# Kernel optimization log

Hardware: AMD Instinct MI355X
Metric: run time of the kernel (lower is better)

## Reference

```python
import jax, jax.numpy as jnp
import numpy as np

U, I, D = 100000, 50000, 64
N = U + I
E_G, E_U, E_I = 2400000, 1600000, 800000


def _spmm(rows, cols, vals, x, n):
    # sparse [n, m] @ dense [m, d] via gather + scale + segment-sum scatter
    return jax.ops.segment_sum(x[cols] * vals[:, None], rows, num_segments=n)


def setup_inputs() -> dict:
    key = jax.random.key(0)
    ks = jax.random.split(key, 11)
    return {
        "user_emb": jax.random.normal(ks[0], (U, D), dtype=jnp.float32),
        "item_emb": jax.random.normal(ks[1], (I, D), dtype=jnp.float32),
        "graph_rows": jax.random.randint(ks[2], (E_G,), 0, N, dtype=jnp.int32),
        "graph_cols": jax.random.randint(ks[3], (E_G,), 0, N, dtype=jnp.int32),
        "graph_vals": jax.random.uniform(ks[4], (E_G,), dtype=jnp.float32),
        "user_rows": jax.random.randint(ks[5], (E_U,), 0, U, dtype=jnp.int32),
        "user_cols": jax.random.randint(ks[6], (E_U,), 0, U, dtype=jnp.int32),
        "user_vals": jax.random.uniform(ks[7], (E_U,), dtype=jnp.float32),
        "item_rows": jax.random.randint(ks[8], (E_I,), 0, I, dtype=jnp.int32),
        "item_cols": jax.random.randint(ks[9], (E_I,), 0, I, dtype=jnp.int32),
        "item_vals": jax.random.uniform(ks[10], (E_I,), dtype=jnp.float32),
    }


def reference(user_emb, item_emb,
              graph_rows, graph_cols, graph_vals,
              user_rows, user_cols, user_vals,
              item_rows, item_cols, item_vals):
    all_emb = jnp.concatenate([user_emb, item_emb], axis=0)  # [N, D]
    all_emb1 = _spmm(graph_rows, graph_cols, graph_vals, all_emb, N)
    user_emb2 = _spmm(user_rows, user_cols, user_vals, user_emb, U)
    item_emb2 = _spmm(item_rows, item_cols, item_vals, item_emb, I)
    user_emb1, item_emb1 = all_emb1[:U], all_emb1[U:]
    return (user_emb1, item_emb1, user_emb2, item_emb2)
```

## Files before the change

kernel.cpp:

```cpp
#include <hip/hip_runtime.h>

#define DDIM 64
constexpr int U_CNT = 100000;
constexpr int I_CNT = 50000;
constexpr int N_CNT = U_CNT + I_CNT;
constexpr int NB    = N_CNT + U_CNT + I_CNT;

constexpr int BIN_ROWS_LOG = 7;
constexpr int BIN_ROWS = 1 << BIN_ROWS_LOG;
constexpr int BINS = (NB + BIN_ROWS - 1) / BIN_ROWS;
constexpr int BINS_PAD = 2560;
constexpr int SORT_EDGES = 4096;
constexpr int HIST_EDGES = 16384;
constexpr int CAP = 2432;
constexpr int CAPH = 1536;
constexpr int NSLOT = 5;

constexpr int SB_LOG = 12;
constexpr int NSB = (NB + (1 << SB_LOG) - 1) >> SB_LOG;
constexpr int NSB_PAD = 128;
constexpr int CAP_SB = 67584;
constexpr int MAXCH = (CAP_SB + SORT_EDGES - 1) / SORT_EDGES;
constexpr int BWIN = 80;
constexpr int BWIN_PAD = 128;

typedef unsigned u32x2 __attribute__((ext_vector_type(2)));
typedef unsigned u32x4 __attribute__((ext_vector_type(4)));
typedef float    f32x2 __attribute__((ext_vector_type(2)));

__device__ __forceinline__ int wave_incl_scan(int v, int lane) {
#pragma unroll
    for (int off = 1; off < 64; off <<= 1) {
        int t = __shfl_up(v, off, 64);
        if (lane >= off) v += t;
    }
    return v;
}

__device__ __forceinline__ unsigned short f2bf_rne(float f) {
    unsigned u = __float_as_uint(f);
    unsigned r = (u + 0x7FFFu + ((u >> 16) & 1u)) >> 16;
    return (unsigned short)r;
}

__global__ __launch_bounds__(1024) void init_cursors(int* __restrict__ sbcur,
                                                     int* __restrict__ bincur) {
    int i = blockIdx.x * 1024 + threadIdx.x;
    if (i < NSB) sbcur[i] = i * CAP_SB;
    if (i < BINS) bincur[i] = i * CAP;
}

__global__ __launch_bounds__(256) void convert_emb(const float* __restrict__ ue,
                                                   const float* __restrict__ ie,
                                                   unsigned short* __restrict__ emb16) {
    int g = blockIdx.x * 256 + threadIdx.x;
    constexpr int UG = U_CNT * (DDIM / 4);
    constexpr int TG = N_CNT * (DDIM / 4);
    if (g >= TG) return;
    float4 v = (g < UG) ? ((const float4*)ue)[g] : ((const float4*)ie)[g - UG];
    ushort4 o;
    o.x = f2bf_rne(v.x); o.y = f2bf_rne(v.y); o.z = f2bf_rne(v.z); o.w = f2bf_rne(v.w);
    ((ushort4*)emb16)[g] = o;
}

__global__ __launch_bounds__(1024) void hist_conv(const int* __restrict__ gr,
                                                  const int* __restrict__ ur,
                                                  const int* __restrict__ ir,
                                                  int EG, int EU, int EI,
                                                  int* __restrict__ cnt,
                                                  const float* __restrict__ ue,
                                                  const float* __restrict__ ie,
                                                  unsigned short* __restrict__ emb16) {
    __shared__ int h[BINS_PAD];
    for (int i = threadIdx.x; i < BINS_PAD; i += 1024) h[i] = 0;
    if (emb16) {
        constexpr int UG = U_CNT * (DDIM / 4);
        constexpr int TG = N_CNT * (DDIM / 4);
        int stride = (int)gridDim.x * 1024;
        for (int g = blockIdx.x * 1024 + threadIdx.x; g < TG; g += stride) {
            float4 v = (g < UG) ? ((const float4*)ue)[g] : ((const float4*)ie)[g - UG];
            ushort4 o;
            o.x = f2bf_rne(v.x); o.y = f2bf_rne(v.y); o.z = f2bf_rne(v.z); o.w = f2bf_rne(v.w);
            ((ushort4*)emb16)[g] = o;
        }
    }
    __syncthreads();
    int base = blockIdx.x * HIST_EDGES;
    int Et = EG + EU + EI;
    for (int j = 0; j < HIST_EDGES / 1024; ++j) {
        int e = base + j * 1024 + threadIdx.x;
        if (e < Et) {
            int b;
            if (e < EG)           b = gr[e];
            else if (e < EG + EU) b = N_CNT + ur[e - EG];
            else                  b = N_CNT + U_CNT + ir[e - EG - EU];
            atomicAdd(&h[b >> BIN_ROWS_LOG], 1);
        }
    }
    __syncthreads();
    for (int i = threadIdx.x; i < BINS; i += 1024) {
        int v = h[i];
        if (v) atomicAdd(&cnt[i], v);
    }
}

__global__ __launch_bounds__(1024) void scan_bins(const int* __restrict__ cnt,
                                                  int* __restrict__ bin_base,
                                                  int* __restrict__ bin_cursor,
                                                  int* __restrict__ sb_base,
                                                  int* __restrict__ sb_cursor,
                                                  int E_total) {
    __shared__ int wsum[16], woff[16];
    int tid = threadIdx.x, lane = tid & 63, wid = tid >> 6;
    int i0 = 3 * tid, i1 = i0 + 1, i2 = i0 + 2;
    int c0 = (i0 < BINS) ? cnt[i0] : 0;
    int c1 = (i1 < BINS) ? cnt[i1] : 0;
    int c2 = (i2 < BINS) ? cnt[i2] : 0;
    int v = c0 + c1 + c2;
    int incl = wave_incl_scan(v, lane);
    if (lane == 63) wsum[wid] = incl;
    __syncthreads();
    if (wid == 0 && lane < 16) {
        int s = wsum[lane], si = s;
#pragma unroll
        for (int off = 1; off < 16; off <<= 1) {
            int t = __shfl_up(si, off, 64);
            if (lane >= off) si += t;
        }
        woff[lane] = si - s;
    }
    __syncthreads();
    int e = incl - v + woff[wid];
    if (i0 < BINS) { bin_base[i0] = e;           bin_cursor[i0] = e; }
    if (i1 < BINS) { bin_base[i1] = e + c0;      bin_cursor[i1] = e + c0; }
    if (i2 < BINS) { bin_base[i2] = e + c0 + c1; bin_cursor[i2] = e + c0 + c1; }
    if (tid == 0) bin_base[BINS] = E_total;
    __syncthreads();
    if (tid <= NSB) {
        int idx = tid << (SB_LOG - BIN_ROWS_LOG);
        int vv = (idx >= BINS) ? E_total : bin_base[idx];
        sb_base[tid] = vv;
        if (tid < NSB) sb_cursor[tid] = vv;
    }
}

__global__ __launch_bounds__(512, 8) void sbsort_all(
        const int* __restrict__ gr, const int* __restrict__ gc, const float* __restrict__ gv,
        const int* __restrict__ ur, const int* __restrict__ uc, const float* __restrict__ uv,
        const int* __restrict__ ir, const int* __restrict__ ic, const float* __restrict__ iv,
        int EG, int EU, int EI,
        int* __restrict__ sb_cursor, uint2* __restrict__ poolA) {
    __shared__ uint2 sorted[SORT_EDGES];
    __shared__ unsigned char ssb[SORT_EDGES];
    __shared__ int hist[NSB_PAD];
    __shared__ int lscan[NSB_PAD];
    __shared__ int lcur[NSB_PAD];
    __shared__ int wsum2[2];

    int tid = threadIdx.x, lane = tid & 63, wid = tid >> 6;
    for (int i = tid; i < NSB_PAD; i += 512) { hist[i] = 0; lcur[i] = 0; }
    __syncthreads();

    const int Et = EG + EU + EI;
    int start = blockIdx.x * SORT_EDGES;
    int base_e = start + tid * 8;
    int myb[8]; unsigned mylo[8]; float myv[8];

#pragma unroll
    for (int j = 0; j < 8; j += 4) {
        int e = base_e + j;
        int sg0 = (e < EG) ? 0 : (e < EG + EU ? 1 : 2);
        int sg3 = (e + 3 < EG) ? 0 : (e + 3 < EG + EU ? 1 : 2);
        if (e + 3 < Et && sg0 == sg3) {
            const int* R; const int* Cc; const float* V; int boff, goff, loc;
            if (sg0 == 0)      { R = gr; Cc = gc; V = gv; boff = 0;             goff = 0;     loc = e; }
            else if (sg0 == 1) { R = ur; Cc = uc; V = uv; boff = N_CNT;         goff = 0;     loc = e - EG; }
            else               { R = ir; Cc = ic; V = iv; boff = N_CNT + U_CNT; goff = U_CNT; loc = e - EG - EU; }
            int4   r4 = *(const int4*)(R + loc);
            int4   c4 = *(const int4*)(Cc + loc);
            float4 v4 = *(const float4*)(V + loc);
            int rr[4] = {r4.x, r4.y, r4.z, r4.w};
            int cc[4] = {c4.x, c4.y, c4.z, c4.w};
            float vv[4] = {v4.x, v4.y, v4.z, v4.w};
#pragma unroll
            for (int q = 0; q < 4; ++q) {
                int bucket = boff + rr[q];
                int sb = bucket >> SB_LOG;
                myb[j + q] = sb;
                mylo[j + q] = ((unsigned)(bucket & 4095) << 18) | (unsigned)(goff + cc[q]);
                myv[j + q] = vv[q];
                atomicAdd(&hist[sb], 1);
            }
        } else {
#pragma unroll
            for (int q = 0; q < 4; ++q) {
                int ee = e + q;
                if (ee < Et) {
                    int r, c; float vl; int boff, goff;
                    if (ee < EG)           { r = gr[ee]; c = gc[ee]; vl = gv[ee]; boff = 0; goff = 0; }
                    else if (ee < EG + EU) { int k = ee - EG;      r = ur[k]; c = uc[k]; vl = uv[k]; boff = N_CNT;         goff = 0; }
                    else                   { int k = ee - EG - EU; r = ir[k]; c = ic[k]; vl = iv[k]; boff = N_CNT + U_CNT; goff = U_CNT; }
                    int bucket = boff + r;
                    int sb = bucket >> SB_LOG;
                    myb[j + q] = sb;
                    mylo[j + q] = ((unsigned)(bucket & 4095) << 18) | (unsigned)(goff + c);
                    myv[j + q] = vl;
                    atomicAdd(&hist[sb], 1);
                } else myb[j + q] = -1;
            }
        }
    }
    __syncthreads();

    int v = 0, incl = 0;
    if (tid < NSB_PAD) {
        v = hist[tid];
        incl = wave_incl_scan(v, lane);
        if (lane == 63) wsum2[wid] = incl;
    }
    __syncthreads();
    if (tid < NSB_PAD) {
        int st = incl - v + (wid ? wsum2[0] : 0);
        lscan[tid] = st;
        if (tid < NSB && v) hist[tid] = atomicAdd(&sb_cursor[tid], v);
    }
    __syncthreads();

#pragma unroll
    for (int j = 0; j < 8; ++j) {
        if (myb[j] >= 0) {
            int p = lscan[myb[j]] + atomicAdd(&lcur[myb[j]], 1);
            sorted[p] = make_uint2(mylo[j], __float_as_uint(myv[j]));
            ssb[p] = (unsigned char)myb[j];
        }
    }
    __syncthreads();

    int cntE = min(SORT_EDGES, Et - start);
    for (int pos = tid; pos < cntE; pos += 512) {
        int b = ssb[pos];
        uint2 t = sorted[pos];
        u32x2 q; q.x = t.x; q.y = t.y;
        __builtin_nontemporal_store(q, (u32x2*)&poolA[hist[b] + (pos - lscan[b])]);
    }
}

__global__ __launch_bounds__(512, 8) void binsort2_fx(const uint2* __restrict__ poolA,
                                                      const int* __restrict__ sbcur,
                                                      int* __restrict__ bincur,
                                                      uint2* __restrict__ poolB) {
    __shared__ uint2 sorted[SORT_EDGES];
    __shared__ unsigned char sbin[SORT_EDGES];
    __shared__ int hist[32], lscan[32], lcur[32];

    int sb = blockIdx.y, c = blockIdx.x;
    int cnt_sb = sbcur[sb] - sb * CAP_SB;
    int lo = c * SORT_EDGES;
    if (lo >= cnt_sb) return;
    int m = min(SORT_EDGES, cnt_sb - lo);

    int tid = threadIdx.x, lane = tid & 63;
    if (tid < 32) hist[tid] = 0;
    __syncthreads();

    const uint2* src = poolA + (size_t)sb * CAP_SB + lo;
    int base = tid * 8;
    int mys[8]; uint2 myp[8];
#pragma unroll
    for (int j = 0; j < 8; j += 2) {
        int e = base + j;
        uint2 p0, p1;
        bool v1 = (e + 1 < m), v0 = (e < m);
        if (v1) {
            u32x4 q = __builtin_nontemporal_load((const u32x4*)(src + e));
            p0.x = q.x; p0.y = q.y; p1.x = q.z; p1.y = q.w;
        } else if (v0) {
            u32x2 q = __builtin_nontemporal_load((const u32x2*)(src + e));
            p0.x = q.x; p0.y = q.y;
        }
        if (v0) {
            int slot = (int)(p0.x >> 25);
            mys[j] = slot; myp[j] = p0;
            atomicAdd(&hist[slot], 1);
        } else mys[j] = -1;
        if (v1) {
            int slot = (int)(p1.x >> 25);
            mys[j + 1] = slot; myp[j + 1] = p1;
            atomicAdd(&hist[slot], 1);
        } else mys[j + 1] = -1;
    }
    __syncthreads();

    if (tid < 64) {
        int vv = (tid < 32) ? hist[tid] : 0;
        int incl = wave_incl_scan(vv, lane);
        if (tid < 32) { lscan[tid] = incl - vv; lcur[tid] = incl - vv; }
    }
    __syncthreads();
    if (tid < 32 && hist[tid] > 0)
        hist[tid] = atomicAdd(&bincur[(sb << 5) + tid], hist[tid]);
    __syncthreads();

#pragma unroll
    for (int j = 0; j < 8; ++j) {
        if (mys[j] >= 0) {
            int p = atomicAdd(&lcur[mys[j]], 1);
            sorted[p] = myp[j];
            sbin[p] = (unsigned char)mys[j];
        }
    }
    __syncthreads();

    for (int pos = tid; pos < m; pos += 512) {
        int sl = sbin[pos];
        uint2 t = sorted[pos];
        u32x2 q; q.x = t.x; q.y = t.y;
        __builtin_nontemporal_store(q, (u32x2*)&poolB[hist[sl] + (pos - lscan[sl])]);
    }
}

__global__ __launch_bounds__(512, 8) void binsort2_win(const uint2* __restrict__ poolA,
                                                       const int* __restrict__ sb_base, int Et,
                                                       int* __restrict__ bin_cursor,
                                                       uint2* __restrict__ poolB) {
    __shared__ uint2 sorted[SORT_EDGES];
    __shared__ unsigned char sbin[SORT_EDGES];
    __shared__ int hist[BWIN_PAD];
    __shared__ int lscan[BWIN_PAD];
    __shared__ int lcur[BWIN_PAD];
    __shared__ int ssbb[NSB + 1];
    __shared__ int wsum2[2];
    __shared__ int sblo_s, nloc;

    int tid = threadIdx.x, lane = tid & 63, wid = tid >> 6;
    if (tid < BWIN_PAD) hist[tid] = 0;
    if (tid <= NSB) ssbb[tid] = sb_base[tid];
    __syncthreads();

    int start = blockIdx.x * SORT_EDGES;
    int base_e = start + tid * 8;
    int sb;
    {
        int lo2 = 0, hi2 = NSB - 1;
        while (lo2 < hi2) {
            int mid = (lo2 + hi2 + 1) >> 1;
            if (ssbb[mid] <= base_e) lo2 = mid; else hi2 = mid - 1;
        }
        sb = lo2;
    }
    if (tid == 0) {
        int lo2 = 0, hi2 = NSB - 1;
        while (lo2 < hi2) {
            int mid = (lo2 + hi2 + 1) >> 1;
            if (ssbb[mid] <= start) lo2 = mid; else hi2 = mid - 1;
        }
        sblo_s = lo2;
    }
    __syncthreads();
    int sb_lo = sblo_s;
    int W0 = sb_lo << (SB_LOG - BIN_ROWS_LOG);

    int myb[8]; uint2 myp[8];
#pragma unroll
    for (int j = 0; j < 8; j += 2) {
        int e = base_e + j;
        uint2 p0, p1;
        bool v1 = (e + 1 < Et), v0 = (e < Et);
        if (v1) {
            u32x4 q = __builtin_nontemporal_load((const u32x4*)(poolA + e));
            p0.x = q.x; p0.y = q.y; p1.x = q.z; p1.y = q.w;
        } else if (v0) {
            u32x2 q = __builtin_nontemporal_load((const u32x2*)(poolA + e));
            p0.x = q.x; p0.y = q.y;
        }
        if (v0) {
            while (sb < NSB - 1 && e >= ssbb[sb + 1]) ++sb;
            int slot = ((sb - sb_lo) << (SB_LOG - BIN_ROWS_LOG)) + (int)(p0.x >> 25);
            if ((unsigned)slot < (unsigned)BWIN) {
                myb[j] = slot; myp[j] = p0;
                atomicAdd(&hist[slot], 1);
            } else {
                int b = (sb << (SB_LOG - BIN_ROWS_LOG)) + (int)(p0.x >> 25);
                int gp = atomicAdd(&bin_cursor[b], 1);
                poolB[gp] = p0;
                myb[j] = -1;
            }
        } else myb[j] = -1;
        if (v1) {
            int e1 = e + 1;
            while (sb < NSB - 1 && e1 >= ssbb[sb + 1]) ++sb;
            int slot = ((sb - sb_lo) << (SB_LOG - BIN_ROWS_LOG)) + (int)(p1.x >> 25);
            if ((unsigned)slot < (unsigned)BWIN) {
                myb[j + 1] = slot; myp[j + 1] = p1;
                atomicAdd(&hist[slot], 1);
            } else {
                int b = (sb << (SB_LOG - BIN_ROWS_LOG)) + (int)(p1.x >> 25);
                int gp = atomicAdd(&bin_cursor[b], 1);
                poolB[gp] = p1;
                myb[j + 1] = -1;
            }
        } else myb[j + 1] = -1;
    }
    __syncthreads();

    int v = 0, incl = 0;
    if (tid < BWIN_PAD) {
        v = hist[tid];
        incl = wave_incl_scan(v, lane);
        if (lane == 63) wsum2[wid] = incl;
    }
    __syncthreads();
    if (tid < BWIN_PAD) {
        int st = incl - v + (wid ? wsum2[0] : 0);
        lscan[tid] = st; lcur[tid] = st;
        if (tid == BWIN_PAD - 1) nloc = st + v;
    }
    __syncthreads();
    if (tid < BWIN && hist[tid] > 0)
        hist[tid] = atomicAdd(&bin_cursor[W0 + tid], hist[tid]);
    __syncthreads();

#pragma unroll
    for (int j = 0; j < 8; ++j) {
        if (myb[j] >= 0) {
            int p = atomicAdd(&lcur[myb[j]], 1);
            sorted[p] = myp[j];
            sbin[p] = (unsigned char)myb[j];
        }
    }
    __syncthreads();

    int tot = nloc;
    for (int pos = tid; pos < tot; pos += 512) {
        int sl = sbin[pos];
        uint2 t = sorted[pos];
        u32x2 q; q.x = t.x; q.y = t.y;
        __builtin_nontemporal_store(q, (u32x2*)&poolB[hist[sl] + (pos - lscan[sl])]);
    }
}

__global__ __launch_bounds__(512, 8) void refine_accum(const int* __restrict__ bin_base,
                                                       const int* __restrict__ bincur,
                                                       const uint2* __restrict__ pool,
                                                       const unsigned short* __restrict__ emb16,
                                                       float* __restrict__ out) {
    __shared__ uint2 sorted[CAPH + 4];
    __shared__ int rhist[BIN_ROWS];
    __shared__ int rstart[BIN_ROWS];
    __shared__ int rcur[BIN_ROWS];
    __shared__ int wsum[2];
    int tid = threadIdx.x, lane = tid & 63, wid = tid >> 6;

    int ix = (int)blockIdx.x;
    int b = ix >> 1;
    int rlo = (ix & 1) << 6, rhi = rlo + 64;

    int s, cnt;
    if (bin_base) { s = bin_base[b]; cnt = min(bin_base[b + 1] - s, CAP); }
    else          { s = b * CAP;     cnt = min(bincur[b] - s, CAP); }

    if (tid < BIN_ROWS) rhist[tid] = 0;
    __syncthreads();

    uint2 my[NSLOT];
    const u32x2* poolv = (const u32x2*)(pool + s);
#pragma unroll
    for (int j = 0; j < NSLOT; ++j) {
        int idx = tid + j * 512;
        if (idx < cnt) {
            u32x2 q = __builtin_nontemporal_load(poolv + idx);
            my[j].x = q.x; my[j].y = q.y;
            int rl = (int)((q.x >> 18) & 127u);
            if (rl >= rlo && rl < rhi) atomicAdd(&rhist[rl], 1);
        }
    }
    __syncthreads();

    int v = 0, incl = 0;
    if (tid < BIN_ROWS) {
        v = rhist[tid];
        incl = wave_incl_scan(v, lane);
        if (lane == 63) wsum[wid] = incl;
    }
    __syncthreads();
    if (tid < BIN_ROWS) {
        int st = incl - v + (wid ? wsum[0] : 0);
        rstart[tid] = st; rcur[tid] = st;
    }
    __syncthreads();

#pragma unroll
    for (int j = 0; j < NSLOT; ++j) {
        int idx = tid + j * 512;
        if (idx < cnt) {
            int rl = (int)((my[j].x >> 18) & 127u);
            if (rl >= rlo && rl < rhi) {
                int pos = atomicAdd(&rcur[rl], 1);
                if (pos < CAPH) sorted[pos] = my[j];
            }
        }
    }
    __syncthreads();
    if (tid == 0) {
        int total = rcur[rhi - 1];
        if (total > CAPH) total = CAPH;
        sorted[total] = make_uint2(0u, 0u);
    }
    __syncthreads();

    long long rowbase = (long long)b * BIN_ROWS;
    int half = lane >> 5, hl = lane & 31;
    const unsigned* emb32 = (const unsigned*)emb16;
    for (int r = rlo + wid; r < rhi; r += 8) {
        long long row = rowbase + r;
        if (row >= NB) break;
        int k = rstart[r], ke = k + rhist[r];
        float a0 = 0.f, a1 = 0.f, c0 = 0.f, c1 = 0.f;
        for (; k + 8 <= ke; k += 8) {
            uint2 p0 = sorted[k + half];
            uint2 p1 = sorted[k + 2 + half];
            uint2 p2 = sorted[k + 4 + half];
            uint2 p3 = sorted[k + 6 + half];
            unsigned w0 = emb32[((size_t)(p0.x & 0x3FFFFu) << 5) + hl];
            unsigned w1 = emb32[((size_t)(p1.x & 0x3FFFFu) << 5) + hl];
            unsigned w2 = emb32[((size_t)(p2.x & 0x3FFFFu) << 5) + hl];
            unsigned w3 = emb32[((size_t)(p3.x & 0x3FFFFu) << 5) + hl];
            float v0 = __uint_as_float(p0.y), v1 = __uint_as_float(p1.y);
            float v2 = __uint_as_float(p2.y), v3 = __uint_as_float(p3.y);
            a0 += v0 * __uint_as_float(w0 << 16);
            a1 += v0 * __uint_as_float(w0 & 0xFFFF0000u);
            c0 += v1 * __uint_as_float(w1 << 16);
            c1 += v1 * __uint_as_float(w1 & 0xFFFF0000u);
            a0 += v2 * __uint_as_float(w2 << 16);
            a1 += v2 * __uint_as_float(w2 & 0xFFFF0000u);
            c0 += v3 * __uint_as_float(w3 << 16);
            c1 += v3 * __uint_as_float(w3 & 0xFFFF0000u);
        }
        for (; k + 2 <= ke; k += 2) {
            uint2 p = sorted[k + half];
            unsigned w = emb32[((size_t)(p.x & 0x3FFFFu) << 5) + hl];
            float vv = __uint_as_float(p.y);
            a0 += vv * __uint_as_float(w << 16);
            a1 += vv * __uint_as_float(w & 0xFFFF0000u);
        }
        if (k < ke) {
            uint2 p = sorted[k + half];
            unsigned w = emb32[((size_t)(p.x & 0x3FFFFu) << 5) + hl];
            float vv = half ? 0.f : __uint_as_float(p.y);
            a0 += vv * __uint_as_float(w << 16);
            a1 += vv * __uint_as_float(w & 0xFFFF0000u);
        }
        a0 += c0; a1 += c1;
        a0 += __shfl_xor(a0, 32, 64);
        a1 += __shfl_xor(a1, 32, 64);
        if (lane < 32) {
            f32x2 o; o.x = a0; o.y = a1;
            __builtin_nontemporal_store(o, (f32x2*)(out + (size_t)row * DDIM + 2 * hl));
        }
    }
}

__global__ void spmm_graph_kernel(const int* __restrict__ rows, const int* __restrict__ cols,
                                  const float* __restrict__ vals,
                                  const float* __restrict__ user_emb,
                                  const float* __restrict__ item_emb,
                                  float* __restrict__ out, int E) {
    long long idx = (long long)blockIdx.x * blockDim.x + threadIdx.x;
    int e = (int)(idx >> 6), d = (int)(idx & 63);
    if (e >= E) return;
    int r = rows[e], c = cols[e];
    float v = vals[e];
    float x = (c < U_CNT) ? user_emb[(long long)c * DDIM + d]
                          : item_emb[(long long)(c - U_CNT) * DDIM + d];
    atomicAdd(&out[(long long)r * DDIM + d], v * x);
}

__global__ void spmm_plain_kernel(const int* __restrict__ rows, const int* __restrict__ cols,
                                  const float* __restrict__ vals,
                                  const float* __restrict__ emb,
                                  float* __restrict__ out, int E) {
    long long idx = (long long)blockIdx.x * blockDim.x + threadIdx.x;
    int e = (int)(idx >> 6), d = (int)(idx & 63);
    if (e >= E) return;
    int r = rows[e], c = cols[e];
    atomicAdd(&out[(long long)r * DDIM + d], vals[e] * emb[(long long)c * DDIM + d]);
}

extern "C" void kernel_launch(void* const* d_in, const int* in_sizes, int n_in,
                              void* d_out, int out_size, void* d_ws, size_t ws_size,
                              hipStream_t stream) {
    const float* user_emb = (const float*)d_in[0];
    const float* item_emb = (const float*)d_in[1];
    const int*   g_rows   = (const int*)d_in[2];
    const int*   g_cols   = (const int*)d_in[3];
    const float* g_vals   = (const float*)d_in[4];
    const int*   u_rows   = (const int*)d_in[5];
    const int*   u_cols   = (const int*)d_in[6];
    const float* u_vals   = (const float*)d_in[7];
    const int*   i_rows   = (const int*)d_in[8];
    const int*   i_cols   = (const int*)d_in[9];
    const float* i_vals   = (const float*)d_in[10];
    float* out = (float*)d_out;

    const int EG = in_sizes[2];
    const int EU = in_sizes[5];
    const int EI = in_sizes[8];
    const int Et = EG + EU + EI;

    const size_t emb_bytes = (size_t)N_CNT * DDIM * sizeof(unsigned short);
    unsigned cgrid = (unsigned)((N_CNT * (DDIM / 4) + 255) / 256);

    size_t f_off_bc  = 80 * sizeof(int);
    size_t f_off_pa  = (f_off_bc + (size_t)BINS * sizeof(int) + 127) & ~(size_t)127;
    size_t f_pa_sz   = (size_t)NSB * CAP_SB * sizeof(uint2);
    size_t f_off_pb  = (f_off_pa + f_pa_sz + 127) & ~(size_t)127;
    size_t f_pb_sz   = (size_t)BINS * CAP * sizeof(uint2);
    size_t needed_fx = f_off_pb + f_pb_sz;

    size_t t_off_bb   = (size_t)BINS_PAD * sizeof(int);
    size_t t_off_bc   = t_off_bb + (size_t)(BINS + 1) * sizeof(int);
    size_t t_off_sbb  = t_off_bc + (size_t)BINS * sizeof(int);
    size_t t_off_sbc  = t_off_sbb + (size_t)(NSB + 1) * sizeof(int);
    size_t t_off_pa   = (t_off_sbc + (size_t)NSB * sizeof(int) + 127) & ~(size_t)127;
    size_t t_off_pb   = (t_off_pa + (size_t)Et * sizeof(uint2) + 127) & ~(size_t)127;
    size_t needed_2p  = t_off_pb + (size_t)Et * sizeof(uint2);
    size_t t_off_emb  = (needed_2p + 127) & ~(size_t)127;
    size_t needed_na  = t_off_emb + emb_bytes;
    bool pa_fits_emb  = (size_t)Et * sizeof(uint2) >= emb_bytes;

    if (ws_size >= needed_fx && f_pa_sz >= emb_bytes) {
        int*   sbcur  = (int*)d_ws;
        int*   bincur = (int*)((char*)d_ws + f_off_bc);
        uint2* poolA  = (uint2*)((char*)d_ws + f_off_pa);
        uint2* poolB  = (uint2*)((char*)d_ws + f_off_pb);
        unsigned short* emb16 = (unsigned short*)poolA;

        init_cursors<<<3, 1024, 0, stream>>>(sbcur, bincur);

        unsigned nb2 = (unsigned)((Et + SORT_EDGES - 1) / SORT_EDGES);
        sbsort_all<<<nb2, 512, 0, stream>>>(g_rows, g_cols, g_vals,
                                            u_rows, u_cols, u_vals,
                                            i_rows, i_cols, i_vals,
                                            EG, EU, EI, sbcur, poolA);
        binsort2_fx<<<dim3(MAXCH, NSB), 512, 0, stream>>>(poolA, sbcur, bincur, poolB);
        convert_emb<<<cgrid, 256, 0, stream>>>(user_emb, item_emb, emb16);
        refine_accum<<<2 * BINS, 512, 0, stream>>>(nullptr, bincur, poolB, emb16, out);
    } else if (ws_size >= needed_2p && pa_fits_emb) {
        bool noalias = (ws_size >= needed_na);
        int*   cnt        = (int*)d_ws;
        int*   bin_base   = (int*)((char*)d_ws + t_off_bb);
        int*   bin_cursor = (int*)((char*)d_ws + t_off_bc);
        int*   sb_base    = (int*)((char*)d_ws + t_off_sbb);
        int*   sb_cursor  = (int*)((char*)d_ws + t_off_sbc);
        uint2* poolA      = (uint2*)((char*)d_ws + t_off_pa);
        uint2* poolB      = (uint2*)((char*)d_ws + t_off_pb);
        unsigned short* emb16 = noalias ? (unsigned short*)((char*)d_ws + t_off_emb)
                                        : (unsigned short*)poolA;

        hipMemsetAsync(cnt, 0, (size_t)BINS_PAD * sizeof(int), stream);
        unsigned hblocks = (unsigned)((Et + HIST_EDGES - 1) / HIST_EDGES);
        hist_conv<<<hblocks, 1024, 0, stream>>>(g_rows, u_rows, i_rows, EG, EU, EI, cnt,
                                                user_emb, item_emb,
                                                noalias ? emb16 : (unsigned short*)nullptr);
        scan_bins<<<1, 1024, 0, stream>>>(cnt, bin_base, bin_cursor, sb_base, sb_cursor, Et);

        unsigned nb2 = (unsigned)((Et + SORT_EDGES - 1) / SORT_EDGES);
        sbsort_all<<<nb2, 512, 0, stream>>>(g_rows, g_cols, g_vals,
                                            u_rows, u_cols, u_vals,
                                            i_rows, i_cols, i_vals,
                                            EG, EU, EI, sb_cursor, poolA);
        binsort2_win<<<nb2, 512, 0, stream>>>(poolA, sb_base, Et, bin_cursor, poolB);

        if (!noalias)
            convert_emb<<<cgrid, 256, 0, stream>>>(user_emb, item_emb, emb16);

        refine_accum<<<2 * BINS, 512, 0, stream>>>(bin_base, nullptr, poolB, emb16, out);
    } else {
        hipMemsetAsync(d_out, 0, (size_t)out_size * sizeof(float), stream);
        const int block = 256;
        {
            long long t = (long long)EG * DDIM;
            spmm_graph_kernel<<<(unsigned)((t + block - 1) / block), block, 0, stream>>>(
                g_rows, g_cols, g_vals, user_emb, item_emb, out, EG);
        }
        {
            long long t = (long long)EU * DDIM;
            spmm_plain_kernel<<<(unsigned)((t + block - 1) / block), block, 0, stream>>>(
                u_rows, u_cols, u_vals, user_emb, out + (size_t)N_CNT * DDIM, EU);
        }
        {
            long long t = (long long)EI * DDIM;
            spmm_plain_kernel<<<(unsigned)((t + block - 1) / block), block, 0, stream>>>(
                i_rows, i_cols, i_vals, item_emb, out + (size_t)(N_CNT + U_CNT) * DDIM, EI);
        }
    }
}
```

Baseline: 323.5 us.

## Fuse bf16 embedding conversion into sort kernel and use 1024-thread blocks

```diff
diff --git a/kernel.cpp b/kernel.cpp
--- a/kernel.cpp
+++ b/kernel.cpp
@@ -13,8 +13,7 @@
 constexpr int SORT_EDGES = 4096;
 constexpr int HIST_EDGES = 16384;
 constexpr int CAP = 2432;
-constexpr int CAPH = 1536;
-constexpr int NSLOT = 5;
+constexpr int NSLOT = 3;
 
 constexpr int SB_LOG = 12;
 constexpr int NSB = (NB + (1 << SB_LOG) - 1) >> SB_LOG;
@@ -144,12 +143,14 @@
     }
 }
 
-__global__ __launch_bounds__(512, 8) void sbsort_all(
+__global__ __launch_bounds__(1024, 8) void sbsort_all(
         const int* __restrict__ gr, const int* __restrict__ gc, const float* __restrict__ gv,
         const int* __restrict__ ur, const int* __restrict__ uc, const float* __restrict__ uv,
         const int* __restrict__ ir, const int* __restrict__ ic, const float* __restrict__ iv,
         int EG, int EU, int EI,
-        int* __restrict__ sb_cursor, uint2* __restrict__ poolA) {
+        int* __restrict__ sb_cursor, uint2* __restrict__ poolA,
+        const float* __restrict__ ue, const float* __restrict__ ie,
+        unsigned short* __restrict__ emb16c) {
     __shared__ uint2 sorted[SORT_EDGES];
     __shared__ unsigned char ssb[SORT_EDGES];
     __shared__ int hist[NSB_PAD];
@@ -158,17 +159,16 @@
     __shared__ int wsum2[2];
 
     int tid = threadIdx.x, lane = tid & 63, wid = tid >> 6;
-    for (int i = tid; i < NSB_PAD; i += 512) { hist[i] = 0; lcur[i] = 0; }
+    if (tid < NSB_PAD) { hist[tid] = 0; lcur[tid] = 0; }
     __syncthreads();
 
     const int Et = EG + EU + EI;
     int start = blockIdx.x * SORT_EDGES;
-    int base_e = start + tid * 8;
-    int myb[8]; unsigned mylo[8]; float myv[8];
-
-#pragma unroll
-    for (int j = 0; j < 8; j += 4) {
-        int e = base_e + j;
+    int base_e = start + tid * 4;
+    int myb[4]; unsigned mylo[4]; float myv[4];
+
+    {
+        int e = base_e;
         int sg0 = (e < EG) ? 0 : (e < EG + EU ? 1 : 2);
         int sg3 = (e + 3 < EG) ? 0 : (e + 3 < EG + EU ? 1 : 2);
         if (e + 3 < Et && sg0 == sg3) {
@@ -186,9 +186,9 @@
             for (int q = 0; q < 4; ++q) {
                 int bucket = boff + rr[q];
                 int sb = bucket >> SB_LOG;
-                myb[j + q] = sb;
-                mylo[j + q] = ((unsigned)(bucket & 4095) << 18) | (unsigned)(goff + cc[q]);
-                myv[j + q] = vv[q];
+                myb[q] = sb;
+                mylo[q] = ((unsigned)(bucket & 4095) << 18) | (unsigned)(goff + cc[q]);
+                myv[q] = vv[q];
                 atomicAdd(&hist[sb], 1);
             }
         } else {
@@ -202,11 +202,11 @@
                     else                   { int k = ee - EG - EU; r = ir[k]; c = ic[k]; vl = iv[k]; boff = N_CNT + U_CNT; goff = U_CNT; }
                     int bucket = boff + r;
                     int sb = bucket >> SB_LOG;
-                    myb[j + q] = sb;
-                    mylo[j + q] = ((unsigned)(bucket & 4095) << 18) | (unsigned)(goff + c);
-                    myv[j + q] = vl;
+                    myb[q] = sb;
+                    mylo[q] = ((unsigned)(bucket & 4095) << 18) | (unsigned)(goff + c);
+                    myv[q] = vl;
                     atomicAdd(&hist[sb], 1);
-                } else myb[j + q] = -1;
+                } else myb[q] = -1;
             }
         }
     }
@@ -227,7 +227,7 @@
     __syncthreads();
 
 #pragma unroll
-    for (int j = 0; j < 8; ++j) {
+    for (int j = 0; j < 4; ++j) {
         if (myb[j] >= 0) {
             int p = lscan[myb[j]] + atomicAdd(&lcur[myb[j]], 1);
             sorted[p] = make_uint2(mylo[j], __float_as_uint(myv[j]));
@@ -237,18 +237,30 @@
     __syncthreads();
 
     int cntE = min(SORT_EDGES, Et - start);
-    for (int pos = tid; pos < cntE; pos += 512) {
+    for (int pos = tid; pos < cntE; pos += 1024) {
         int b = ssb[pos];
         uint2 t = sorted[pos];
         u32x2 q; q.x = t.x; q.y = t.y;
         __builtin_nontemporal_store(q, (u32x2*)&poolA[hist[b] + (pos - lscan[b])]);
     }
-}
-
-__global__ __launch_bounds__(512, 8) void binsort2_fx(const uint2* __restrict__ poolA,
-                                                      const int* __restrict__ sbcur,
-                                                      int* __restrict__ bincur,
-                                                      uint2* __restrict__ poolB) {
+
+    if (emb16c) {
+        constexpr int UG = U_CNT * (DDIM / 4);
+        constexpr int TG = N_CNT * (DDIM / 4);
+        int stride = (int)gridDim.x * 1024;
+        for (int g = blockIdx.x * 1024 + tid; g < TG; g += stride) {
+            float4 vv = (g < UG) ? ((const float4*)ue)[g] : ((const float4*)ie)[g - UG];
+            ushort4 o;
+            o.x = f2bf_rne(vv.x); o.y = f2bf_rne(vv.y); o.z = f2bf_rne(vv.z); o.w = f2bf_rne(vv.w);
+            ((ushort4*)emb16c)[g] = o;
+        }
+    }
+}
+
+__global__ __launch_bounds__(1024, 8) void binsort2_fx(const uint2* __restrict__ poolA,
+                                                       const int* __restrict__ sbcur,
+                                                       int* __restrict__ bincur,
+                                                       uint2* __restrict__ poolB) {
     __shared__ uint2 sorted[SORT_EDGES];
     __shared__ unsigned char sbin[SORT_EDGES];
     __shared__ int hist[32], lscan[32], lcur[32];
@@ -264,10 +276,10 @@
     __syncthreads();
 
     const uint2* src = poolA + (size_t)sb * CAP_SB + lo;
-    int base = tid * 8;
-    int mys[8]; uint2 myp[8];
-#pragma unroll
-    for (int j = 0; j < 8; j += 2) {
+    int base = tid * 4;
+    int mys[4]; uint2 myp[4];
+#pragma unroll
+    for (int j = 0; j < 4; j += 2) {
         int e = base + j;
         uint2 p0, p1;
         bool v1 = (e + 1 < m), v0 = (e < m);
@@ -302,7 +314,7 @@
     __syncthreads();
 
 #pragma unroll
-    for (int j = 0; j < 8; ++j) {
+    for (int j = 0; j < 4; ++j) {
         if (mys[j] >= 0) {
             int p = atomicAdd(&lcur[mys[j]], 1);
             sorted[p] = myp[j];
@@ -311,7 +323,7 @@
     }
     __syncthreads();
 
-    for (int pos = tid; pos < m; pos += 512) {
+    for (int pos = tid; pos < m; pos += 1024) {
         int sl = sbin[pos];
         uint2 t = sorted[pos];
         u32x2 q; q.x = t.x; q.y = t.y;
@@ -439,22 +451,19 @@
     }
 }
 
-__global__ __launch_bounds__(512, 8) void refine_accum(const int* __restrict__ bin_base,
-                                                       const int* __restrict__ bincur,
-                                                       const uint2* __restrict__ pool,
-                                                       const unsigned short* __restrict__ emb16,
-                                                       float* __restrict__ out) {
-    __shared__ uint2 sorted[CAPH + 4];
+__global__ __launch_bounds__(1024, 8) void refine_accum(const int* __restrict__ bin_base,
+                                                        const int* __restrict__ bincur,
+                                                        const uint2* __restrict__ pool,
+                                                        const unsigned short* __restrict__ emb16,
+                                                        float* __restrict__ out) {
+    __shared__ uint2 sorted[CAP + 2];
     __shared__ int rhist[BIN_ROWS];
     __shared__ int rstart[BIN_ROWS];
     __shared__ int rcur[BIN_ROWS];
     __shared__ int wsum[2];
     int tid = threadIdx.x, lane = tid & 63, wid = tid >> 6;
 
-    int ix = (int)blockIdx.x;
-    int b = ix >> 1;
-    int rlo = (ix & 1) << 6, rhi = rlo + 64;
-
+    int b = (int)blockIdx.x;
     int s, cnt;
     if (bin_base) { s = bin_base[b]; cnt = min(bin_base[b + 1] - s, CAP); }
     else          { s = b * CAP;     cnt = min(bincur[b] - s, CAP); }
@@ -466,12 +475,11 @@
     const u32x2* poolv = (const u32x2*)(pool + s);
 #pragma unroll
     for (int j = 0; j < NSLOT; ++j) {
-        int idx = tid + j * 512;
+        int idx = tid + j * 1024;
         if (idx < cnt) {
             u32x2 q = __builtin_nontemporal_load(poolv + idx);
             my[j].x = q.x; my[j].y = q.y;
-            int rl = (int)((q.x >> 18) & 127u);
-            if (rl >= rlo && rl < rhi) atomicAdd(&rhist[rl], 1);
+            atomicAdd(&rhist[(q.x >> 18) & 127u], 1);
         }
     }
     __syncthreads();
@@ -491,27 +499,20 @@
 
 #pragma unroll
     for (int j = 0; j < NSLOT; ++j) {
-        int idx = tid + j * 512;
+        int idx = tid + j * 1024;
         if (idx < cnt) {
-            int rl = (int)((my[j].x >> 18) & 127u);
-            if (rl >= rlo && rl < rhi) {
-                int pos = atomicAdd(&rcur[rl], 1);
-                if (pos < CAPH) sorted[pos] = my[j];
-            }
-        }
-    }
-    __syncthreads();
-    if (tid == 0) {
-        int total = rcur[rhi - 1];
-        if (total > CAPH) total = CAPH;
-        sorted[total] = make_uint2(0u, 0u);
-    }
+            int pos = atomicAdd(&rcur[(my[j].x >> 18) & 127u], 1);
+            sorted[pos] = my[j];
+        }
+    }
+    __syncthreads();
+    if (tid == 0) sorted[cnt] = make_uint2(0u, 0u);
     __syncthreads();
 
     long long rowbase = (long long)b * BIN_ROWS;
     int half = lane >> 5, hl = lane & 31;
     const unsigned* emb32 = (const unsigned*)emb16;
-    for (int r = rlo + wid; r < rhi; r += 8) {
+    for (int r = wid; r < BIN_ROWS; r += 16) {
         long long row = rowbase + r;
         if (row >= NB) break;
         int k = rstart[r], ke = k + rhist[r];
@@ -610,12 +611,17 @@
     const size_t emb_bytes = (size_t)N_CNT * DDIM * sizeof(unsigned short);
     unsigned cgrid = (unsigned)((N_CNT * (DDIM / 4) + 255) / 256);
 
-    size_t f_off_bc  = 80 * sizeof(int);
-    size_t f_off_pa  = (f_off_bc + (size_t)BINS * sizeof(int) + 127) & ~(size_t)127;
-    size_t f_pa_sz   = (size_t)NSB * CAP_SB * sizeof(uint2);
-    size_t f_off_pb  = (f_off_pa + f_pa_sz + 127) & ~(size_t)127;
-    size_t f_pb_sz   = (size_t)BINS * CAP * sizeof(uint2);
-    size_t needed_fx = f_off_pb + f_pb_sz;
+    size_t f_off_bc   = 80 * sizeof(int);
+    size_t f_hdr_end  = f_off_bc + (size_t)BINS * sizeof(int);
+    size_t f_pa_sz    = (size_t)NSB * CAP_SB * sizeof(uint2);
+    size_t f_pb_sz    = (size_t)BINS * CAP * sizeof(uint2);
+    size_t f_off_pa_a = (f_hdr_end + 127) & ~(size_t)127;
+    size_t f_off_pb_a = (f_off_pa_a + f_pa_sz + 127) & ~(size_t)127;
+    size_t needed_fa  = f_off_pb_a + f_pb_sz;
+    size_t f_off_emb  = (f_hdr_end + 127) & ~(size_t)127;
+    size_t f_off_pa_n = (f_off_emb + emb_bytes + 127) & ~(size_t)127;
+    size_t f_off_pb_n = (f_off_pa_n + f_pa_sz + 127) & ~(size_t)127;
+    size_t needed_fn  = f_off_pb_n + f_pb_sz;
 
     size_t t_off_bb   = (size_t)BINS_PAD * sizeof(int);
     size_t t_off_bc   = t_off_bb + (size_t)(BINS + 1) * sizeof(int);
@@ -628,23 +634,28 @@
     size_t needed_na  = t_off_emb + emb_bytes;
     bool pa_fits_emb  = (size_t)Et * sizeof(uint2) >= emb_bytes;
 
-    if (ws_size >= needed_fx && f_pa_sz >= emb_bytes) {
+    if (ws_size >= needed_fa && f_pa_sz >= emb_bytes) {
+        bool noalias = (ws_size >= needed_fn);
         int*   sbcur  = (int*)d_ws;
         int*   bincur = (int*)((char*)d_ws + f_off_bc);
-        uint2* poolA  = (uint2*)((char*)d_ws + f_off_pa);
-        uint2* poolB  = (uint2*)((char*)d_ws + f_off_pb);
-        unsigned short* emb16 = (unsigned short*)poolA;
+        uint2* poolA  = (uint2*)((char*)d_ws + (noalias ? f_off_pa_n : f_off_pa_a));
+        uint2* poolB  = (uint2*)((char*)d_ws + (noalias ? f_off_pb_n : f_off_pb_a));
+        unsigned short* emb16 = noalias ? (unsigned short*)((char*)d_ws + f_off_emb)
+                                        : (unsigned short*)poolA;
 
         init_cursors<<<3, 1024, 0, stream>>>(sbcur, bincur);
 
         unsigned nb2 = (unsigned)((Et + SORT_EDGES - 1) / SORT_EDGES);
-        sbsort_all<<<nb2, 512, 0, stream>>>(g_rows, g_cols, g_vals,
-                                            u_rows, u_cols, u_vals,
-                                            i_rows, i_cols, i_vals,
-                                            EG, EU, EI, sbcur, poolA);
-        binsort2_fx<<<dim3(MAXCH, NSB), 512, 0, stream>>>(poolA, sbcur, bincur, poolB);
-        convert_emb<<<cgrid, 256, 0, stream>>>(user_emb, item_emb, emb16);
-        refine_accum<<<2 * BINS, 512, 0, stream>>>(nullptr, bincur, poolB, emb16, out);
+        sbsort_all<<<nb2, 1024, 0, stream>>>(g_rows, g_cols, g_vals,
+                                             u_rows, u_cols, u_vals,
+                                             i_rows, i_cols, i_vals,
+                                             EG, EU, EI, sbcur, poolA,
+                                             user_emb, item_emb,
+                                             noalias ? emb16 : (unsigned short*)nullptr);
+        binsort2_fx<<<dim3(MAXCH, NSB), 1024, 0, stream>>>(poolA, sbcur, bincur, poolB);
+        if (!noalias)
+            convert_emb<<<cgrid, 256, 0, stream>>>(user_emb, item_emb, emb16);
+        refine_accum<<<BINS, 1024, 0, stream>>>(nullptr, bincur, poolB, emb16, out);
     } else if (ws_size >= needed_2p && pa_fits_emb) {
         bool noalias = (ws_size >= needed_na);
         int*   cnt        = (int*)d_ws;
@@ -665,16 +676,18 @@
         scan_bins<<<1, 1024, 0, stream>>>(cnt, bin_base, bin_cursor, sb_base, sb_cursor, Et);
 
         unsigned nb2 = (unsigned)((Et + SORT_EDGES - 1) / SORT_EDGES);
-        sbsort_all<<<nb2, 512, 0, stream>>>(g_rows, g_cols, g_vals,
-                                            u_rows, u_cols, u_vals,
-                                            i_rows, i_cols, i_vals,
-                                            EG, EU, EI, sb_cursor, poolA);
+        sbsort_all<<<nb2, 1024, 0, stream>>>(g_rows, g_cols, g_vals,
+                                             u_rows, u_cols, u_vals,
+                                             i_rows, i_cols, i_vals,
+                                             EG, EU, EI, sb_cursor, poolA,
+                                             (const float*)nullptr, (const float*)nullptr,
+                                             (unsigned short*)nullptr);
         binsort2_win<<<nb2, 512, 0, stream>>>(poolA, sb_base, Et, bin_cursor, poolB);
 
         if (!noalias)
             convert_emb<<<cgrid, 256, 0, stream>>>(user_emb, item_emb, emb16);
 
-        refine_accum<<<2 * BINS, 512, 0, stream>>>(bin_base, nullptr, poolB, emb16, out);
+        refine_accum<<<BINS, 1024, 0, stream>>>(bin_base, nullptr, poolB, emb16, out);
     } else {
         hipMemsetAsync(d_out, 0, (size_t)out_size * sizeof(float), stream);
         const int block = 256;
```

Measured after the change: 305.5 us. 5.6% less time.
